# Kernel tuning notes

Hardware: AMD Instinct MI355X
Metric: run time of the kernel (lower is better)

## Reference

```python
import jax, jax.numpy as jnp
import numpy as np

IN_FEATS = 16
OUT_FEATS = 16
EDGE_FEATS = 16
N_NODES = 50000
N_EDGES = 800000


def setup_inputs() -> dict:
    key = jax.random.key(0)
    k = jax.random.split(key, 7)
    feat = jax.random.normal(k[0], (N_NODES, IN_FEATS), dtype=jnp.float32)
    efeat = jax.random.normal(k[1], (N_EDGES, EDGE_FEATS), dtype=jnp.float32)
    # edge_nn = Linear(EDGE_FEATS, IN_FEATS*OUT_FEATS)
    We = jax.random.normal(k[2], (EDGE_FEATS, IN_FEATS * OUT_FEATS), dtype=jnp.float32) * 0.1
    be = jax.random.normal(k[3], (IN_FEATS * OUT_FEATS,), dtype=jnp.float32) * 0.1
    bias = jax.random.normal(k[4], (OUT_FEATS,), dtype=jnp.float32) * 0.1
    src = jax.random.randint(k[5], (N_EDGES,), 0, N_NODES, dtype=jnp.int64 if jax.config.jax_enable_x64 else jnp.int32)
    dst = jnp.sort(jax.random.randint(k[6], (N_EDGES,), 0, N_NODES, dtype=jnp.int64 if jax.config.jax_enable_x64 else jnp.int32))
    return {"feat": feat, "efeat": efeat, "We": We, "be": be, "bias": bias,
            "src": src, "dst": dst, "num_nodes": N_NODES}


def reference(feat, efeat, We, be, bias, src, dst, num_nodes):
    # edge-conditioned weights: [E, in, out]
    w = (efeat @ We + be).reshape(-1, IN_FEATS, OUT_FEATS)
    # gather source features and per-edge matvec: sum_i h_src[e,i] * w[e,i,o]
    m = jnp.einsum('ei,eio->eo', feat[src], w)  # [E, out]
    # segment-sum aggregation to destination nodes ('sum' reducer)
    neigh = jax.ops.segment_sum(m, dst, num_segments=num_nodes)  # [N, out]
    # residual (Identity since in_feats == out_feats) + bias
    return neigh + feat + bias
```

## Files before the change

### kernel.cpp

```cpp
#include <hip/hip_runtime.h>
#include <hip/hip_bf16.h>

typedef __attribute__((ext_vector_type(2))) _Float16 half2v;
typedef __attribute__((ext_vector_type(8))) _Float16 half8v;
typedef __attribute__((ext_vector_type(4))) float f32x4;

#define NBLK 2048
#define WT (NBLK * 4)

__global__ __launch_bounds__(256) void setup_kernel(
    const float* __restrict__ feat, const float* __restrict__ bias,
    const float* __restrict__ We, const float* __restrict__ be,
    float* __restrict__ out, unsigned short* __restrict__ wp,
    int n_elems, int initB) {
  if ((int)blockIdx.x < initB) {
    int g = blockIdx.x * 256 + threadIdx.x;
    int base = g * 4;
    if (base < n_elems) {
      float4 f = *reinterpret_cast<const float4*>(feat + base);
      const float4* b4 = reinterpret_cast<const float4*>(bias);
      float4 b = b4[g & 3];
      float4 o;
      o.x = f.x + b.x; o.y = f.y + b.y; o.z = f.z + b.z; o.w = f.w + b.w;
      *reinterpret_cast<float4*>(out + base) = o;
    }
  } else {
    int idx = (blockIdx.x - initB) * 256 + threadIdx.x;
    if (idx < 9 * 4 * 16 * 8) {
      int j = idx & 7, n = (idx >> 3) & 15, gg = (idx >> 7) & 3, t = idx >> 9;
      float v = 0.f;
      if (t < 8) {
        int c = (gg >> 1) * 8 + t;
        int i = (gg & 1) * 8 + j;
        v = We[c * 256 + i * 16 + n];
      } else if (gg < 2) {
        v = be[(gg * 8 + j) * 16 + n];
      }
      _Float16 hv = (_Float16)v;
      wp[idx] = __builtin_bit_cast(unsigned short, hv);
    }
  }
}

__device__ __forceinline__ void compute_tile(
    float4 E0, float4 E1, float4 H0, float4 H1, int4 dd,
    int g, int m, const half8v* Bf, float* __restrict__ out) {
  half2v ef2[4], h2[4];
  ef2[0] = half2v{(_Float16)E0.x, (_Float16)E0.y};
  ef2[1] = half2v{(_Float16)E0.z, (_Float16)E0.w};
  ef2[2] = half2v{(_Float16)E1.x, (_Float16)E1.y};
  ef2[3] = half2v{(_Float16)E1.z, (_Float16)E1.w};
  h2[0]  = half2v{(_Float16)H0.x, (_Float16)H0.y};
  h2[1]  = half2v{(_Float16)H0.z, (_Float16)H0.w};
  h2[2]  = half2v{(_Float16)H1.x, (_Float16)H1.y};
  h2[3]  = half2v{(_Float16)H1.z, (_Float16)H1.w};

  f32x4 accA = {0.f, 0.f, 0.f, 0.f};
  f32x4 accB = {0.f, 0.f, 0.f, 0.f};
#pragma unroll
  for (int t = 0; t < 8; ++t) {
    _Float16 ev = ef2[t >> 1][t & 1];
    half2v evb = half2v{ev, ev};
    half2v a0 = evb * h2[0], a1 = evb * h2[1], a2 = evb * h2[2], a3 = evb * h2[3];
    half8v A;
    A[0] = a0[0]; A[1] = a0[1]; A[2] = a1[0]; A[3] = a1[1];
    A[4] = a2[0]; A[5] = a2[1]; A[6] = a3[0]; A[7] = a3[1];
    if (t & 1)
      accB = __builtin_amdgcn_mfma_f32_16x16x32_f16(A, Bf[t], accB, 0, 0, 0);
    else
      accA = __builtin_amdgcn_mfma_f32_16x16x32_f16(A, Bf[t], accA, 0, 0, 0);
  }
  {
    half2v z = half2v{(_Float16)0.f, (_Float16)0.f};
    half2v b0 = (g < 2) ? h2[0] : z, b1 = (g < 2) ? h2[1] : z;
    half2v b2 = (g < 2) ? h2[2] : z, b3 = (g < 2) ? h2[3] : z;
    half8v A;
    A[0] = b0[0]; A[1] = b0[1]; A[2] = b1[0]; A[3] = b1[1];
    A[4] = b2[0]; A[5] = b2[1]; A[6] = b3[0]; A[7] = b3[1];
    accB = __builtin_amdgcn_mfma_f32_16x16x32_f16(A, Bf[8], accB, 0, 0, 0);
  }
  f32x4 acc;
  acc[0] = accA[0] + accB[0]; acc[1] = accA[1] + accB[1];
  acc[2] = accA[2] + accB[2]; acc[3] = accA[3] + accB[3];

  float run = acc[0];
  int cur = dd.x;
  if (dd.y == cur) run += acc[1];
  else { unsafeAtomicAdd(out + (size_t)cur * 16 + m, run); cur = dd.y; run = acc[1]; }
  if (dd.z == cur) run += acc[2];
  else { unsafeAtomicAdd(out + (size_t)cur * 16 + m, run); cur = dd.z; run = acc[2]; }
  if (dd.w == cur) run += acc[3];
  else { unsafeAtomicAdd(out + (size_t)cur * 16 + m, run); cur = dd.w; run = acc[3]; }
  unsafeAtomicAdd(out + (size_t)cur * 16 + m, run);
}

__global__ __launch_bounds__(256) void edge_mfma_kernel(
    const float* __restrict__ feat, const float* __restrict__ efeat,
    const int* __restrict__ src, const int* __restrict__ dst,
    const unsigned short* __restrict__ wp,
    float* __restrict__ out, int E) {
  int wave = blockIdx.x * 4 + (threadIdx.x >> 6);
  int lane = threadIdx.x & 63;
  int g = lane >> 4;
  int m = lane & 15;
  int p = g >> 1;
  int hh = g & 1;

  int ntiles = (E + 15) >> 4;
  if (wave >= ntiles) return;
  const bool partialF = (E & 15) != 0;
  const int lastT = ntiles - 1;

  half8v Bf[9];
#pragma unroll
  for (int t = 0; t < 9; ++t)
    Bf[t] = *reinterpret_cast<const half8v*>(wp + (unsigned)(t * 64 + lane) * 8);

  const float4* ef4 = reinterpret_cast<const float4*>(efeat);
  const float4* f4  = reinterpret_cast<const float4*>(feat);
  const int4*   d4  = reinterpret_cast<const int4*>(dst);

  int tile = wave;
  float4 E0, E1, H0, H1;
  int4 dd;
  if (__builtin_expect(partialF && tile == lastT, 0)) {
    int e = tile * 16 + m;
    int ec = min(e, E - 1);
    E0 = ef4[(unsigned)ec * 4 + p * 2]; E1 = ef4[(unsigned)ec * 4 + p * 2 + 1];
    if (e >= E) { E0 = make_float4(0.f,0.f,0.f,0.f); E1 = E0; }
    int s = src[ec];
    H0 = f4[(unsigned)s * 4 + hh * 2]; H1 = f4[(unsigned)s * 4 + hh * 2 + 1];
    if (e >= E) { H0 = make_float4(0.f,0.f,0.f,0.f); H1 = H0; }
    int b = tile * 16 + g * 4;
    dd.x = dst[min(b + 0, E - 1)]; dd.y = dst[min(b + 1, E - 1)];
    dd.z = dst[min(b + 2, E - 1)]; dd.w = dst[min(b + 3, E - 1)];
  } else {
    int e = tile * 16 + m;
    int s = src[e];
    E0 = ef4[(unsigned)e * 4 + p * 2]; E1 = ef4[(unsigned)e * 4 + p * 2 + 1];
    dd = d4[(unsigned)tile * 4 + g];
    H0 = f4[(unsigned)s * 4 + hh * 2]; H1 = f4[(unsigned)s * 4 + hh * 2 + 1];
  }

  int tile1 = tile + WT;
  int s1 = 0;
  if (tile1 < ntiles) s1 = src[min(tile1 * 16 + m, E - 1)];

  while (tile1 < ntiles) {
    int tile2 = tile1 + WT;

    float4 E0n, E1n, H0n, H1n;
    int4 ddn;
    if (__builtin_expect(partialF && tile1 == lastT, 0)) {
      int e = tile1 * 16 + m;
      int ec = min(e, E - 1);
      E0n = ef4[(unsigned)ec * 4 + p * 2]; E1n = ef4[(unsigned)ec * 4 + p * 2 + 1];
      if (e >= E) { E0n = make_float4(0.f,0.f,0.f,0.f); E1n = E0n; }
      int b = tile1 * 16 + g * 4;
      ddn.x = dst[min(b + 0, E - 1)]; ddn.y = dst[min(b + 1, E - 1)];
      ddn.z = dst[min(b + 2, E - 1)]; ddn.w = dst[min(b + 3, E - 1)];
    } else {
      int e = tile1 * 16 + m;
      E0n = ef4[(unsigned)e * 4 + p * 2]; E1n = ef4[(unsigned)e * 4 + p * 2 + 1];
      ddn = d4[(unsigned)tile1 * 4 + g];
    }
    H0n = f4[(unsigned)s1 * 4 + hh * 2]; H1n = f4[(unsigned)s1 * 4 + hh * 2 + 1];
    int s2 = src[min(tile2 * 16 + m, E - 1)];

    __builtin_amdgcn_sched_barrier(0);

    compute_tile(E0, E1, H0, H1, dd, g, m, Bf, out);

    E0 = E0n; E1 = E1n; H0 = H0n; H1 = H1n; dd = ddn; s1 = s2;
    tile = tile1; tile1 = tile2;
  }

  compute_tile(E0, E1, H0, H1, dd, g, m, Bf, out);
}

extern "C" void kernel_launch(void* const* d_in, const int* in_sizes, int n_in,
                              void* d_out, int out_size, void* d_ws, size_t ws_size,
                              hipStream_t stream) {
  const float* feat  = (const float*)d_in[0];
  const float* efeat = (const float*)d_in[1];
  const float* We    = (const float*)d_in[2];
  const float* be    = (const float*)d_in[3];
  const float* bias  = (const float*)d_in[4];
  const int*   src   = (const int*)d_in[5];
  const int*   dst   = (const int*)d_in[6];
  float* out = (float*)d_out;

  int E = in_sizes[5];
  int n_elems = out_size;

  int groups = (n_elems + 3) / 4;
  int initB = (groups + 255) / 256;
  int prepB = (9 * 4 * 16 * 8 + 255) / 256;
  setup_kernel<<<initB + prepB, 256, 0, stream>>>(feat, bias, We, be, out,
                                                  (unsigned short*)d_ws, n_elems, initB);

  int ntiles = (E + 15) / 16;
  int blocks = min(NBLK, (ntiles + 3) / 4);
  edge_mfma_kernel<<<blocks, 256, 0, stream>>>(feat, efeat, src, dst,
                                               (const unsigned short*)d_ws, out, E);
}
```

Measured before the change: 49.93 us.

## Partition tiles per XCD and collapse atomics when a tile shares one destination

Tiles are split into eight contiguous ranges, one per XCD, inferred from blockIdx modulo 8. Each XCD's waves stride within its own range, so neighbouring destination rows stay in that XCD's L2 and atomics to them are less likely to contend across XCDs. A fast path also checks whether all 16 edges in a tile share the same destination node. If so, it reduces across lanes with shuffles and issues one atomic per output column instead of up to four per lane group. The risks are that the XCD mapping assumption may not hold, the grid is now fixed at 2048 blocks regardless of E, and the extra shuffles cost time when the fast path is not taken.

```diff
diff --git a/kernel.cpp b/kernel.cpp
--- a/kernel.cpp
+++ b/kernel.cpp
@@ -6,7 +6,6 @@
 typedef __attribute__((ext_vector_type(4))) float f32x4;
 
 #define NBLK 2048
-#define WT (NBLK * 4)
 
 __global__ __launch_bounds__(256) void setup_kernel(
     const float* __restrict__ feat, const float* __restrict__ bias,
@@ -83,6 +82,16 @@
   acc[0] = accA[0] + accB[0]; acc[1] = accA[1] + accB[1];
   acc[2] = accA[2] + accB[2]; acc[3] = accA[3] + accB[3];
 
+  int nA = __shfl(dd.x, 0, 64);
+  int nB = __shfl(dd.w, 48, 64);
+  if (nA == nB) {
+    float v = acc[0] + acc[1] + acc[2] + acc[3];
+    v += __shfl_xor(v, 32, 64);
+    v += __shfl_xor(v, 16, 64);
+    if (g == 0) unsafeAtomicAdd(out + (size_t)nA * 16 + m, v);
+    return;
+  }
+
   float run = acc[0];
   int cur = dd.x;
   if (dd.y == cur) run += acc[1];
@@ -99,7 +108,7 @@
     const int* __restrict__ src, const int* __restrict__ dst,
     const unsigned short* __restrict__ wp,
     float* __restrict__ out, int E) {
-  int wave = blockIdx.x * 4 + (threadIdx.x >> 6);
+  int wid = threadIdx.x >> 6;
   int lane = threadIdx.x & 63;
   int g = lane >> 4;
   int m = lane & 15;
@@ -107,9 +116,18 @@
   int hh = g & 1;
 
   int ntiles = (E + 15) >> 4;
-  if (wave >= ntiles) return;
   const bool partialF = (E & 15) != 0;
   const int lastT = ntiles - 1;
+
+  int T8 = (ntiles + 7) >> 3;
+  int xcd = blockIdx.x & 7;
+  int wic = (blockIdx.x >> 3) * 4 + wid;
+  int CW = (gridDim.x >> 3) * 4;
+  int cs = xcd * T8;
+  int ce = min(cs + T8, ntiles);
+
+  int tile = cs + wic;
+  if (tile >= ce) return;
 
   half8v Bf[9];
 #pragma unroll
@@ -120,7 +138,6 @@
   const float4* f4  = reinterpret_cast<const float4*>(feat);
   const int4*   d4  = reinterpret_cast<const int4*>(dst);
 
-  int tile = wave;
   float4 E0, E1, H0, H1;
   int4 dd;
   if (__builtin_expect(partialF && tile == lastT, 0)) {
@@ -142,12 +159,12 @@
     H0 = f4[(unsigned)s * 4 + hh * 2]; H1 = f4[(unsigned)s * 4 + hh * 2 + 1];
   }
 
-  int tile1 = tile + WT;
+  int tile1 = tile + CW;
   int s1 = 0;
-  if (tile1 < ntiles) s1 = src[min(tile1 * 16 + m, E - 1)];
-
-  while (tile1 < ntiles) {
-    int tile2 = tile1 + WT;
+  if (tile1 < ce) s1 = src[min(tile1 * 16 + m, E - 1)];
+
+  while (tile1 < ce) {
+    int tile2 = tile1 + CW;
 
     float4 E0n, E1n, H0n, H1n;
     int4 ddn;
@@ -199,8 +216,6 @@
   setup_kernel<<<initB + prepB, 256, 0, stream>>>(feat, bias, We, be, out,
                                                   (unsigned short*)d_ws, n_elems, initB);
 
-  int ntiles = (E + 15) / 16;
-  int blocks = min(NBLK, (ntiles + 3) / 4);
-  edge_mfma_kernel<<<blocks, 256, 0, stream>>>(feat, efeat, src, dst,
-                                               (const unsigned short*)d_ws, out, E);
-}
+  edge_mfma_kernel<<<NBLK, 256, 0, stream>>>(feat, efeat, src, dst,
+                                             (const unsigned short*)d_ws, out, E);
+}
```

Result: faster. 47.48 us (-4.9%).

## Replace atomic scatter with fp16 message buffer and CSR segment-sum kernel

Applied to the files above, without the earlier changes.

Instead of atomically accumulating per-edge messages into the output, the edge kernel writes fp16 messages to a workspace buffer. A setup pass binary-searches the sorted dst to build row pointers, and a new segment-sum kernel reduces each node's messages and adds the residual and bias. This removes atomic contention and the separate output init, at the cost of an extra round trip of message traffic through memory, an extra launch, and fp16 rounding of the messages.

```diff
diff --git a/kernel.cpp b/kernel.cpp
--- a/kernel.cpp
+++ b/kernel.cpp
@@ -1,5 +1,4 @@
 #include <hip/hip_runtime.h>
-#include <hip/hip_bf16.h>
 
 typedef __attribute__((ext_vector_type(2))) _Float16 half2v;
 typedef __attribute__((ext_vector_type(8))) _Float16 half8v;
@@ -7,44 +6,46 @@
 
 #define NBLK 2048
 #define WT (NBLK * 4)
+#define WP_ELEMS (9 * 4 * 16 * 8)
+#define RP_OFF 16384
+#define MS_OFF (16384 + 262144)
 
 __global__ __launch_bounds__(256) void setup_kernel(
-    const float* __restrict__ feat, const float* __restrict__ bias,
     const float* __restrict__ We, const float* __restrict__ be,
-    float* __restrict__ out, unsigned short* __restrict__ wp,
-    int n_elems, int initB) {
-  if ((int)blockIdx.x < initB) {
-    int g = blockIdx.x * 256 + threadIdx.x;
-    int base = g * 4;
-    if (base < n_elems) {
-      float4 f = *reinterpret_cast<const float4*>(feat + base);
-      const float4* b4 = reinterpret_cast<const float4*>(bias);
-      float4 b = b4[g & 3];
-      float4 o;
-      o.x = f.x + b.x; o.y = f.y + b.y; o.z = f.z + b.z; o.w = f.w + b.w;
-      *reinterpret_cast<float4*>(out + base) = o;
+    const int* __restrict__ dst,
+    unsigned short* __restrict__ wp, int* __restrict__ rp,
+    int E, int N) {
+  int idx = blockIdx.x * 256 + threadIdx.x;
+  if (idx < WP_ELEMS) {
+    int j = idx & 7, n = (idx >> 3) & 15, gg = (idx >> 7) & 3, t = idx >> 9;
+    float v = 0.f;
+    if (t < 8) {
+      int c = (gg >> 1) * 8 + t;
+      int i = (gg & 1) * 8 + j;
+      v = We[c * 256 + i * 16 + n];
+    } else if (gg < 2) {
+      v = be[(gg * 8 + j) * 16 + n];
     }
-  } else {
-    int idx = (blockIdx.x - initB) * 256 + threadIdx.x;
-    if (idx < 9 * 4 * 16 * 8) {
-      int j = idx & 7, n = (idx >> 3) & 15, gg = (idx >> 7) & 3, t = idx >> 9;
-      float v = 0.f;
-      if (t < 8) {
-        int c = (gg >> 1) * 8 + t;
-        int i = (gg & 1) * 8 + j;
-        v = We[c * 256 + i * 16 + n];
-      } else if (gg < 2) {
-        v = be[(gg * 8 + j) * 16 + n];
-      }
-      _Float16 hv = (_Float16)v;
-      wp[idx] = __builtin_bit_cast(unsigned short, hv);
+    _Float16 hv = (_Float16)v;
+    wp[idx] = __builtin_bit_cast(unsigned short, hv);
+  }
+  if (idx <= N) {
+    int lo = 0, hi = E;
+    while (lo < hi) {
+      int mid = (lo + hi) >> 1;
+      if (dst[mid] < idx) lo = mid + 1; else hi = mid;
     }
+    rp[idx] = lo;
   }
 }
 
-__device__ __forceinline__ void compute_tile(
-    float4 E0, float4 E1, float4 H0, float4 H1, int4 dd,
-    int g, int m, const half8v* Bf, float* __restrict__ out) {
+__device__ __forceinline__ void compute_store(
+    unsigned short* __restrict__ ms, int tile,
+    float4 E0, float4 E1, float4 H0, float4 H1, bool valid,
+    int g, int lane, const half8v* Bf) {
+  if (!valid) {
+    E0 = make_float4(0.f, 0.f, 0.f, 0.f); E1 = E0; H0 = E0; H1 = E0;
+  }
   half2v ef2[4], h2[4];
   ef2[0] = half2v{(_Float16)E0.x, (_Float16)E0.y};
   ef2[1] = half2v{(_Float16)E0.z, (_Float16)E0.w};
@@ -79,37 +80,25 @@
     A[4] = b2[0]; A[5] = b2[1]; A[6] = b3[0]; A[7] = b3[1];
     accB = __builtin_amdgcn_mfma_f32_16x16x32_f16(A, Bf[8], accB, 0, 0, 0);
   }
-  f32x4 acc;
-  acc[0] = accA[0] + accB[0]; acc[1] = accA[1] + accB[1];
-  acc[2] = accA[2] + accB[2]; acc[3] = accA[3] + accB[3];
-
-  float run = acc[0];
-  int cur = dd.x;
-  if (dd.y == cur) run += acc[1];
-  else { unsafeAtomicAdd(out + (size_t)cur * 16 + m, run); cur = dd.y; run = acc[1]; }
-  if (dd.z == cur) run += acc[2];
-  else { unsafeAtomicAdd(out + (size_t)cur * 16 + m, run); cur = dd.z; run = acc[2]; }
-  if (dd.w == cur) run += acc[3];
-  else { unsafeAtomicAdd(out + (size_t)cur * 16 + m, run); cur = dd.w; run = acc[3]; }
-  unsafeAtomicAdd(out + (size_t)cur * 16 + m, run);
+  half2v lo = half2v{(_Float16)(accA[0] + accB[0]), (_Float16)(accA[1] + accB[1])};
+  half2v hi = half2v{(_Float16)(accA[2] + accB[2]), (_Float16)(accA[3] + accB[3])};
+  uint2 w;
+  w.x = __builtin_bit_cast(unsigned, lo);
+  w.y = __builtin_bit_cast(unsigned, hi);
+  *reinterpret_cast<uint2*>(ms + (size_t)tile * 256 + lane * 4) = w;
 }
 
-__global__ __launch_bounds__(256) void edge_mfma_kernel(
+__global__ __launch_bounds__(256) void edge_gemm_kernel(
     const float* __restrict__ feat, const float* __restrict__ efeat,
-    const int* __restrict__ src, const int* __restrict__ dst,
-    const unsigned short* __restrict__ wp,
-    float* __restrict__ out, int E) {
+    const int* __restrict__ src, const unsigned short* __restrict__ wp,
+    unsigned short* __restrict__ ms, int E) {
   int wave = blockIdx.x * 4 + (threadIdx.x >> 6);
   int lane = threadIdx.x & 63;
-  int g = lane >> 4;
-  int m = lane & 15;
-  int p = g >> 1;
-  int hh = g & 1;
+  int g = lane >> 4, m = lane & 15;
+  int p = g >> 1, hh = g & 1;
 
   int ntiles = (E + 15) >> 4;
   if (wave >= ntiles) return;
-  const bool partialF = (E & 15) != 0;
-  const int lastT = ntiles - 1;
 
   half8v Bf[9];
 #pragma unroll
@@ -118,64 +107,65 @@
 
   const float4* ef4 = reinterpret_cast<const float4*>(efeat);
   const float4* f4  = reinterpret_cast<const float4*>(feat);
-  const int4*   d4  = reinterpret_cast<const int4*>(dst);
 
   int tile = wave;
-  float4 E0, E1, H0, H1;
-  int4 dd;
-  if (__builtin_expect(partialF && tile == lastT, 0)) {
-    int e = tile * 16 + m;
-    int ec = min(e, E - 1);
-    E0 = ef4[(unsigned)ec * 4 + p * 2]; E1 = ef4[(unsigned)ec * 4 + p * 2 + 1];
-    if (e >= E) { E0 = make_float4(0.f,0.f,0.f,0.f); E1 = E0; }
-    int s = src[ec];
-    H0 = f4[(unsigned)s * 4 + hh * 2]; H1 = f4[(unsigned)s * 4 + hh * 2 + 1];
-    if (e >= E) { H0 = make_float4(0.f,0.f,0.f,0.f); H1 = H0; }
-    int b = tile * 16 + g * 4;
-    dd.x = dst[min(b + 0, E - 1)]; dd.y = dst[min(b + 1, E - 1)];
-    dd.z = dst[min(b + 2, E - 1)]; dd.w = dst[min(b + 3, E - 1)];
-  } else {
-    int e = tile * 16 + m;
-    int s = src[e];
-    E0 = ef4[(unsigned)e * 4 + p * 2]; E1 = ef4[(unsigned)e * 4 + p * 2 + 1];
-    dd = d4[(unsigned)tile * 4 + g];
-    H0 = f4[(unsigned)s * 4 + hh * 2]; H1 = f4[(unsigned)s * 4 + hh * 2 + 1];
-  }
-
+  int e0 = tile * 16 + m;
+  bool v_cur = e0 < E;
+  int ec0 = min(e0, E - 1);
+  float4 E0 = ef4[(unsigned)ec0 * 4 + p * 2];
+  float4 E1 = ef4[(unsigned)ec0 * 4 + p * 2 + 1];
+  int s0 = src[ec0];
+  float4 H0 = f4[(unsigned)s0 * 4 + hh * 2];
+  float4 H1 = f4[(unsigned)s0 * 4 + hh * 2 + 1];
   int tile1 = tile + WT;
-  int s1 = 0;
-  if (tile1 < ntiles) s1 = src[min(tile1 * 16 + m, E - 1)];
+  int s1 = (tile1 < ntiles) ? src[min(tile1 * 16 + m, E - 1)] : 0;
 
   while (tile1 < ntiles) {
     int tile2 = tile1 + WT;
-
-    float4 E0n, E1n, H0n, H1n;
-    int4 ddn;
-    if (__builtin_expect(partialF && tile1 == lastT, 0)) {
-      int e = tile1 * 16 + m;
-      int ec = min(e, E - 1);
-      E0n = ef4[(unsigned)ec * 4 + p * 2]; E1n = ef4[(unsigned)ec * 4 + p * 2 + 1];
-      if (e >= E) { E0n = make_float4(0.f,0.f,0.f,0.f); E1n = E0n; }
-      int b = tile1 * 16 + g * 4;
-      ddn.x = dst[min(b + 0, E - 1)]; ddn.y = dst[min(b + 1, E - 1)];
-      ddn.z = dst[min(b + 2, E - 1)]; ddn.w = dst[min(b + 3, E - 1)];
-    } else {
-      int e = tile1 * 16 + m;
-      E0n = ef4[(unsigned)e * 4 + p * 2]; E1n = ef4[(unsigned)e * 4 + p * 2 + 1];
-      ddn = d4[(unsigned)tile1 * 4 + g];
-    }
-    H0n = f4[(unsigned)s1 * 4 + hh * 2]; H1n = f4[(unsigned)s1 * 4 + hh * 2 + 1];
+    int e1 = tile1 * 16 + m;
+    int ec1 = min(e1, E - 1);
+    float4 E0n = ef4[(unsigned)ec1 * 4 + p * 2];
+    float4 E1n = ef4[(unsigned)ec1 * 4 + p * 2 + 1];
+    float4 H0n = f4[(unsigned)s1 * 4 + hh * 2];
+    float4 H1n = f4[(unsigned)s1 * 4 + hh * 2 + 1];
     int s2 = src[min(tile2 * 16 + m, E - 1)];
-
+    bool v_n = e1 < E;
     __builtin_amdgcn_sched_barrier(0);
 
-    compute_tile(E0, E1, H0, H1, dd, g, m, Bf, out);
+    compute_store(ms, tile, E0, E1, H0, H1, v_cur, g, lane, Bf);
 
-    E0 = E0n; E1 = E1n; H0 = H0n; H1 = H1n; dd = ddn; s1 = s2;
+    E0 = E0n; E1 = E1n; H0 = H0n; H1 = H1n; s1 = s2; v_cur = v_n;
     tile = tile1; tile1 = tile2;
   }
+  compute_store(ms, tile, E0, E1, H0, H1, v_cur, g, lane, Bf);
+}
 
-  compute_tile(E0, E1, H0, H1, dd, g, m, Bf, out);
+__device__ __forceinline__ float ms_at(const unsigned short* ms, int e, int c) {
+  unsigned short u = ms[((e >> 4) << 8) + (((e >> 2) & 3) << 6) + (c << 2) + (e & 3)];
+  return (float)__builtin_bit_cast(_Float16, u);
+}
+
+__global__ __launch_bounds__(256) void segsum_kernel(
+    const float* __restrict__ feat, const float* __restrict__ bias,
+    const unsigned short* __restrict__ ms, const int* __restrict__ rp,
+    float* __restrict__ out, int N) {
+  int n = blockIdx.x * 16 + (threadIdx.x >> 4);
+  int c = threadIdx.x & 15;
+  if (n >= N) return;
+  int lo = rp[n], hi = rp[n + 1];
+  float sum = 0.f;
+  int e = lo;
+  while (e < hi && (e & 3)) { sum += ms_at(ms, e, c); ++e; }
+  while (e + 4 <= hi) {
+    const uint2 v = *reinterpret_cast<const uint2*>(
+        ms + ((e >> 4) << 8) + (((e >> 2) & 3) << 6) + (c << 2));
+    half2v x = __builtin_bit_cast(half2v, v.x);
+    half2v y = __builtin_bit_cast(half2v, v.y);
+    sum += (float)x[0] + (float)x[1] + (float)y[0] + (float)y[1];
+    e += 4;
+  }
+  while (e < hi) { sum += ms_at(ms, e, c); ++e; }
+  out[n * 16 + c] = sum + feat[n * 16 + c] + bias[c];
 }
 
 extern "C" void kernel_launch(void* const* d_in, const int* in_sizes, int n_in,
@@ -191,16 +181,19 @@
   float* out = (float*)d_out;
 
   int E = in_sizes[5];
-  int n_elems = out_size;
+  int N = out_size / 16;
 
-  int groups = (n_elems + 3) / 4;
-  int initB = (groups + 255) / 256;
-  int prepB = (9 * 4 * 16 * 8 + 255) / 256;
-  setup_kernel<<<initB + prepB, 256, 0, stream>>>(feat, bias, We, be, out,
-                                                  (unsigned short*)d_ws, n_elems, initB);
+  unsigned short* wp = (unsigned short*)d_ws;
+  int* rp = (int*)((char*)d_ws + RP_OFF);
+  unsigned short* ms = (unsigned short*)((char*)d_ws + MS_OFF);
+
+  int setup_items = (N + 1) > WP_ELEMS ? (N + 1) : WP_ELEMS;
+  setup_kernel<<<(setup_items + 255) / 256, 256, 0, stream>>>(We, be, dst, wp, rp, E, N);
 
   int ntiles = (E + 15) / 16;
-  int blocks = min(NBLK, (ntiles + 3) / 4);
-  edge_mfma_kernel<<<blocks, 256, 0, stream>>>(feat, efeat, src, dst,
-                                               (const unsigned short*)d_ws, out, E);
+  int blocksA = min(NBLK, (ntiles + 3) / 4);
+  edge_gemm_kernel<<<blocksA, 256, 0, stream>>>(feat, efeat, src, wp, ms, E);
+
+  int blocksB = (N + 15) / 16;
+  segsum_kernel<<<blocksB, 256, 0, stream>>>(feat, bias, ms, rp, out, N);
 }
```

New measurement: 43.70 us. 12.5% less time.
